# Performance work log

Measured on AMD Instinct MI355X. Metric: run time of the kernel, lower is better.

The kernel has to match this reference:

```python
import jax, jax.numpy as jnp
import numpy as np

ALPHA = 0.2  # LeakyReLU negative slope for GAT attention
NEG_INF = -1e9


def setup_inputs() -> dict:
    key = jax.random.key(0)
    ks = jax.random.split(key, 10)
    B, N = 8, 1024
    D_vis, D_lab = 512, 256
    H, F = 8, 64            # n_heads, out_per_head -> gat output dim 512
    D_in = D_vis + D_lab    # 768
    D_gat = H * F           # 512
    D_emb = 512

    visual_features = jax.random.normal(ks[0], (B, D_vis), dtype=jnp.float32)
    labels_features = jax.random.normal(ks[1], (N, D_lab), dtype=jnp.float32)
    adj = (jax.random.uniform(ks[2], (N, N)) < 0.1).astype(jnp.float32)
    label_adj_matrix = jnp.maximum(adj, jnp.eye(N, dtype=jnp.float32))

    s = 1.0 / np.sqrt(D_in)
    W = jax.random.uniform(ks[3], (D_in, H, F), minval=-s, maxval=s, dtype=jnp.float32)
    sa = 1.0 / np.sqrt(F)
    a_src = jax.random.uniform(ks[4], (H, F), minval=-sa, maxval=sa, dtype=jnp.float32)
    a_dst = jax.random.uniform(ks[5], (H, F), minval=-sa, maxval=sa, dtype=jnp.float32)
    sq = 1.0 / np.sqrt(D_gat)
    pool_q = jax.random.uniform(ks[6], (D_gat,), minval=-sq, maxval=sq, dtype=jnp.float32)
    fc_W = jax.random.uniform(ks[7], (D_gat, D_emb), minval=-sq, maxval=sq, dtype=jnp.float32)
    fc_b = jax.random.uniform(ks[8], (D_emb,), minval=-sq, maxval=sq, dtype=jnp.float32)

    return {
        "visual_features": visual_features,
        "labels_features": labels_features,
        "label_adj_matrix": label_adj_matrix,
        "W": W, "a_src": a_src, "a_dst": a_dst,
        "pool_q": pool_q, "fc_W": fc_W, "fc_b": fc_b,
    }


def gat_layer(x, adj, W, a_src, a_dst):
    """Multi-head GAT (concat heads). x: (B,N,Din), adj: (N,N)."""
    B, N, _ = x.shape
    H, F = a_src.shape
    Wh = jnp.einsum('bni,ihf->bnhf', x, W)              # (B,N,H,F)
    e_src = jnp.einsum('bnhf,hf->bnh', Wh, a_src)       # (B,N,H)
    e_dst = jnp.einsum('bnhf,hf->bnh', Wh, a_dst)       # (B,N,H)
    e = e_src[:, :, None, :] + e_dst[:, None, :, :]     # (B,N,N,H)
    e = jnp.where(e > 0, e, ALPHA * e)                  # LeakyReLU
    mask = (adj > 0)[None, :, :, None]                  # (1,N,N,1)
    e = jnp.where(mask, e, NEG_INF)
    att = jax.nn.softmax(e, axis=2)                     # over neighbors j
    out = jnp.einsum('bnjh,bjhf->bnhf', att, Wh)        # aggregate
    out = out.reshape(B, N, H * F)
    return jax.nn.elu(out)                              # concat_heads=True -> elu


def reference(visual_features, labels_features, label_adj_matrix,
              W, a_src, a_dst, pool_q, fc_W, fc_b):
    B = visual_features.shape[0]
    N = labels_features.shape[0]
    # per-batch node features: [label_feat || global visual feat]
    lab = jnp.broadcast_to(labels_features[None], (B, N, labels_features.shape[1]))
    vis = jnp.broadcast_to(visual_features[:, None, :], (B, N, visual_features.shape[1]))
    x = jnp.concatenate([lab, vis], axis=-1)            # (B,N,D_in)

    x = gat_layer(x, label_adj_matrix, W, a_src, a_dst) # (B,N,H*F)

    # attention pooling over nodes
    scores = jnp.einsum('bnd,d->bn', x, pool_q)         # (B,N)
    w = jax.nn.softmax(scores, axis=1)
    pooled = jnp.einsum('bn,bnd->bd', w, x)             # (B,D_gat)

    return pooled @ fc_W + fc_b                         # (B,final_embedding_dim)
```

## Files before the change

### kernel.cpp

```cpp
#include <hip/hip_runtime.h>
#include <hip/hip_bf16.h>

#define NN 1024
#define BB 8
#define HH 8
#define FF 64
#define HF 512
#define KT 128

typedef unsigned short ushortT;

__device__ __forceinline__ ushortT f2bf(float f) {
    __hip_bfloat16 h = __float2bfloat16(f);
    return *(ushortT*)&h;
}
__device__ __forceinline__ float bf2f_u(ushortT u) {
    return __uint_as_float((unsigned)u << 16);
}

__global__ void __launch_bounds__(256) k_prep(
    const float* __restrict__ lab, const float* __restrict__ vis,
    const float* __restrict__ adj, const float* __restrict__ Wm,
    const float* __restrict__ a_src, const float* __restrict__ a_dst,
    ushortT* __restrict__ whb, float* __restrict__ whv2, float* __restrict__ bvp,
    float* __restrict__ es, float* __restrict__ ed, float* __restrict__ edT,
    int* __restrict__ list, int* __restrict__ cnt, float* __restrict__ outp)
{
    int bx = blockIdx.x, t = threadIdx.x;
    __shared__ float sh[1024];
    __shared__ float whs[1024];
    if (bx < 512) {
        int np = bx >> 1, ch = bx & 1, n0 = np * 4;
        #pragma unroll
        for (int nd = 0; nd < 4; ++nd)
            sh[nd * 256 + t] = lab[(n0 + nd) * 256 + t];
        __syncthreads();
        float a0 = 0.f, a1 = 0.f, a2 = 0.f, a3 = 0.f;
        const float* wp = Wm + ch * 256 + t;
        #pragma unroll 8
        for (int i = 0; i < 256; ++i) {
            float w = wp[(size_t)i * HF];
            a0 += sh[i] * w;
            a1 += sh[256 + i] * w;
            a2 += sh[512 + i] * w;
            a3 += sh[768 + i] * w;
        }
        int cb = ch * 256 + t;
        whb[(size_t)(n0 + 0) * HF + cb] = f2bf(a0);
        whb[(size_t)(n0 + 1) * HF + cb] = f2bf(a1);
        whb[(size_t)(n0 + 2) * HF + cb] = f2bf(a2);
        whb[(size_t)(n0 + 3) * HF + cb] = f2bf(a3);
        whs[t] = a0; whs[256 + t] = a1; whs[512 + t] = a2; whs[768 + t] = a3;
        __syncthreads();
        if (t < 32) {
            int nd = t >> 3, rest = t & 7, hl = rest >> 1, sd = rest & 1;
            int h = ch * 4 + hl;
            const float* av = (sd ? a_dst : a_src) + h * FF;
            const float* wr = whs + nd * 256 + hl * FF;
            float s = 0.f;
            #pragma unroll
            for (int f = 0; f < FF; ++f) s += wr[f] * av[f];
            int n = n0 + nd;
            if (sd) { ed[n * HH + h] = s; edT[h * NN + n] = s; }
            else es[n * HH + h] = s;
        }
    } else if (bx < 528) {
        int id = bx - 512, b = id >> 1, kh = id & 1;
        if (t < 256) sh[t] = vis[b * 512 + kh * 256 + t];
        __syncthreads();
        float a0 = 0.f, a1 = 0.f;
        const float* wp = Wm + (size_t)(256 + kh * 256) * HF;
        #pragma unroll 4
        for (int i = 0; i < 256; ++i) {
            float xv = sh[i];
            a0 += xv * wp[(size_t)i * HF + t];
            a1 += xv * wp[(size_t)i * HF + t + 256];
        }
        float* dst = whv2 + (size_t)(kh * BB + b) * HF;
        dst[t] = a0; dst[t + 256] = a1;
        whs[t] = a0; whs[256 + t] = a1;
        __syncthreads();
        if (t < 8) {
            const float* as = a_src + t * FF;
            const float* ad = a_dst + t * FF;
            const float* wr = whs + t * FF;
            float s = 0.f;
            #pragma unroll 8
            for (int f = 0; f < FF; ++f) s += wr[f] * (as[f] + ad[f]);
            bvp[kh * 64 + b * 8 + t] = s;
        }
    } else if (bx < 784) {
        int id = bx - 528;
        int i = id * 4 + (t >> 6), lane = t & 63;
        int base = 0;
        for (int c = 0; c < 16; ++c) {
            int j = c * 64 + lane;
            bool pres = adj[(size_t)i * NN + j] > 0.f;
            unsigned long long m = __ballot(pres);
            int pos = __popcll(m & ((1ull << lane) - 1ull));
            if (pres) list[i * NN + base + pos] = j;
            base += __popcll(m);
        }
        if (lane == 0) cnt[i] = base;
    } else {
        float4 z; z.x = 0.f; z.y = 0.f; z.z = 0.f; z.w = 0.f;
        float4* oo = (float4*)outp;
        #pragma unroll
        for (int q = 0; q < 4; ++q) oo[q * 256 + t] = z;
    }
}

__global__ void __launch_bounds__(256) k_attn(
    const ushortT* __restrict__ whb, const float* __restrict__ whv2,
    const float* __restrict__ es, const float* __restrict__ ed,
    const float* __restrict__ edT, const float* __restrict__ bvp,
    const int* __restrict__ list, const int* __restrict__ cnt,
    const float* __restrict__ pool_q,
    ushortT* __restrict__ xoutb, float* __restrict__ sch)
{
    int i = blockIdx.x, z = blockIdx.y, t = threadIdx.x;
    int nn = cnt[i];

    __shared__ float att[KT * 32];
    __shared__ int jl[KT];
    __shared__ float base_s[32], M_s[32], inv_s[32];
    __shared__ float red[8][32];
    __shared__ float edmax_z[4];

    {
        int hl = t >> 6, h = z * 4 + hl;
        const float* col = edT + h * NN;
        float m = -1e30f;
        #pragma unroll
        for (int g = 0; g < 16; ++g) m = fmaxf(m, col[(t & 63) + g * 64]);
        #pragma unroll
        for (int off = 32; off > 0; off >>= 1) m = fmaxf(m, __shfl_down(m, off));
        if ((t & 63) == 0) edmax_z[hl] = m;
    }
    __syncthreads();
    if (t < 32) {
        int hl = t >> 3, b = t & 7, h = z * 4 + hl;
        float base = es[i * HH + h] + bvp[b * 8 + h] + bvp[64 + b * 8 + h];
        base_s[t] = base;
        float mv = base + edmax_z[hl];
        M_s[t] = mv > 0.f ? mv : 0.2f * mv;
    }
    __syncthreads();

    int p = t & 31;
    int hp = z * 4 + (p >> 3);
    float basev = base_s[p], Mv = M_s[p];
    float ssum = 0.f;

    int wid = t >> 6, tf = t & 63;
    int f0 = z * 256 + 4 * tf;
    int hl8 = (tf >> 4) * 8;
    float ac[32];
    #pragma unroll
    for (int q = 0; q < 32; ++q) ac[q] = 0.f;

    for (int c0 = 0; c0 < nn; c0 += KT) {
        int kc = min(KT, nn - c0);
        __syncthreads();
        if (t < kc) jl[t] = list[(size_t)i * NN + c0 + t];
        __syncthreads();
        for (int k = t >> 5; k < kc; k += 8) {
            int j = jl[k];
            float e = basev + ed[j * HH + hp];
            e = e > 0.f ? e : 0.2f * e;
            float pe = __expf(e - Mv);
            ssum += pe;
            att[k * 32 + p] = pe;
        }
        __syncthreads();
        {
            ushort4 u0; u0.x = 0; u0.y = 0; u0.z = 0; u0.w = 0;
            ushort4 u1 = u0;
            if (wid < kc)     u0 = *(const ushort4*)&whb[(size_t)jl[wid] * HF + f0];
            if (wid + 4 < kc) u1 = *(const ushort4*)&whb[(size_t)jl[wid + 4] * HF + f0];
            for (int k = wid; k < kc; k += 4) {
                ushort4 u2 = u1;
                if (k + 8 < kc) u2 = *(const ushort4*)&whb[(size_t)jl[k + 8] * HF + f0];
                float r0 = bf2f_u(u0.x), r1 = bf2f_u(u0.y);
                float r2 = bf2f_u(u0.z), r3 = bf2f_u(u0.w);
                const float4 aA = *(const float4*)&att[k * 32 + hl8];
                const float4 aB = *(const float4*)&att[k * 32 + hl8 + 4];
                ac[0]  += aA.x * r0; ac[8]  += aA.x * r1; ac[16] += aA.x * r2; ac[24] += aA.x * r3;
                ac[1]  += aA.y * r0; ac[9]  += aA.y * r1; ac[17] += aA.y * r2; ac[25] += aA.y * r3;
                ac[2]  += aA.z * r0; ac[10] += aA.z * r1; ac[18] += aA.z * r2; ac[26] += aA.z * r3;
                ac[3]  += aA.w * r0; ac[11] += aA.w * r1; ac[19] += aA.w * r2; ac[27] += aA.w * r3;
                ac[4]  += aB.x * r0; ac[12] += aB.x * r1; ac[20] += aB.x * r2; ac[28] += aB.x * r3;
                ac[5]  += aB.y * r0; ac[13] += aB.y * r1; ac[21] += aB.y * r2; ac[29] += aB.y * r3;
                ac[6]  += aB.z * r0; ac[14] += aB.z * r1; ac[22] += aB.z * r2; ac[30] += aB.z * r3;
                ac[7]  += aB.w * r0; ac[15] += aB.w * r1; ac[23] += aB.w * r2; ac[31] += aB.w * r3;
                u0 = u1; u1 = u2;
            }
        }
    }

    __syncthreads();
    red[t >> 5][p] = ssum;
    float* mrg = att;
    if (wid == 3) {
        #pragma unroll
        for (int q = 0; q < 32; ++q) mrg[q * 64 + tf] = ac[q];
    }
    __syncthreads();
    if (t < 32) {
        float s = 0.f;
        #pragma unroll
        for (int g = 0; g < 8; ++g) s += red[g][t];
        inv_s[t] = 1.0f / s;
    }
    if (wid == 2) {
        #pragma unroll
        for (int q = 0; q < 32; ++q) mrg[q * 64 + tf] += ac[q];
    }
    __syncthreads();
    if (wid == 1) {
        #pragma unroll
        for (int q = 0; q < 32; ++q) mrg[q * 64 + tf] += ac[q];
    }
    __syncthreads();

    if (wid == 0) {
        #pragma unroll
        for (int q = 0; q < 32; ++q) ac[q] += mrg[q * 64 + tf];
        int hl = tf >> 4;
        const float4 pq4 = *(const float4*)&pool_q[f0];
        #pragma unroll
        for (int b = 0; b < BB; ++b) {
            float iv = inv_s[hl * 8 + b];
            const float4 wva = *(const float4*)&whv2[(size_t)b * HF + f0];
            const float4 wvb = *(const float4*)&whv2[(size_t)(BB + b) * HF + f0];
            float o0 = ac[b]      * iv + wva.x + wvb.x;
            float o1 = ac[8 + b]  * iv + wva.y + wvb.y;
            float o2 = ac[16 + b] * iv + wva.z + wvb.z;
            float o3 = ac[24 + b] * iv + wva.w + wvb.w;
            o0 = o0 > 0.f ? o0 : (__expf(o0) - 1.f);
            o1 = o1 > 0.f ? o1 : (__expf(o1) - 1.f);
            o2 = o2 > 0.f ? o2 : (__expf(o2) - 1.f);
            o3 = o3 > 0.f ? o3 : (__expf(o3) - 1.f);
            ushort4 ov;
            ov.x = f2bf(o0); ov.y = f2bf(o1); ov.z = f2bf(o2); ov.w = f2bf(o3);
            *(ushort4*)&xoutb[((size_t)b * NN + i) * HF + f0] = ov;
            float sp = o0 * pq4.x + o1 * pq4.y + o2 * pq4.z + o3 * pq4.w;
            #pragma unroll
            for (int off = 32; off > 0; off >>= 1) sp += __shfl_down(sp, off);
            if (t == 0) sch[(z * BB + b) * NN + i] = sp;
        }
    }
}

__global__ void __launch_bounds__(256) k_tail(const float* __restrict__ sch,
    const ushortT* __restrict__ xoutb, const float* __restrict__ fcW,
    const float* __restrict__ fcb, float* __restrict__ out)
{
    int q = blockIdx.x, b = blockIdx.y, t = threadIdx.x;
    int lane = t & 63, wid = t >> 6;
    __shared__ float red[4];
    __shared__ float sM, sI;
    __shared__ float wl[NN];
    __shared__ float part[16][16];
    __shared__ float pl[16];

    float v[4], e[4];
    float mx = -1e30f;
    #pragma unroll
    for (int qq = 0; qq < 4; ++qq) {
        int n = qq * 256 + t;
        v[qq] = sch[b * NN + n] + sch[(BB + b) * NN + n];
        mx = fmaxf(mx, v[qq]);
    }
    #pragma unroll
    for (int off = 32; off > 0; off >>= 1) mx = fmaxf(mx, __shfl_down(mx, off));
    if (lane == 0) red[wid] = mx;
    __syncthreads();
    if (t == 0) sM = fmaxf(fmaxf(red[0], red[1]), fmaxf(red[2], red[3]));
    __syncthreads();
    float sMv = sM;
    float sm = 0.f;
    #pragma unroll
    for (int qq = 0; qq < 4; ++qq) { e[qq] = __expf(v[qq] - sMv); sm += e[qq]; }
    #pragma unroll
    for (int off = 32; off > 0; off >>= 1) sm += __shfl_down(sm, off);
    __syncthreads();
    if (lane == 0) red[wid] = sm;
    __syncthreads();
    if (t == 0) sI = 1.0f / (red[0] + red[1] + red[2] + red[3]);
    __syncthreads();
    float sIv = sI;
    #pragma unroll
    for (int qq = 0; qq < 4; ++qq) wl[qq * 256 + t] = e[qq] * sIv;
    __syncthreads();

    int fl = t & 15, ng = t >> 4;
    const ushortT* xb = xoutb + (size_t)b * NN * HF + q * 16 + fl;
    float acc0 = 0.f, acc1 = 0.f;
    #pragma unroll 8
    for (int n0 = 0; n0 < NN; n0 += 32) {
        int na = n0 + ng, nb2 = n0 + 16 + ng;
        acc0 += wl[na]  * bf2f_u(xb[(size_t)na  * HF]);
        acc1 += wl[nb2] * bf2f_u(xb[(size_t)nb2 * HF]);
    }
    part[ng][fl] = acc0 + acc1;
    __syncthreads();
    if (t < 16) {
        float s = 0.f;
        #pragma unroll
        for (int g = 0; g < 16; ++g) s += part[g][t];
        pl[t] = s;
    }
    __syncthreads();

    int f0 = 2 * t;
    float ax = 0.f, ay = 0.f;
    if (q == 0) { ax = fcb[f0]; ay = fcb[f0 + 1]; }
    #pragma unroll
    for (int kk = 0; kk < 16; ++kk) {
        float pv = pl[kk];
        const float2 w2 = *(const float2*)&fcW[(size_t)(q * 16 + kk) * HF + f0];
        ax += pv * w2.x; ay += pv * w2.y;
    }
    atomicAdd(&out[b * HF + f0], ax);
    atomicAdd(&out[b * HF + f0 + 1], ay);
}

extern "C" void kernel_launch(void* const* d_in, const int* in_sizes, int n_in,
                              void* d_out, int out_size, void* d_ws, size_t ws_size,
                              hipStream_t stream) {
    const float* vis   = (const float*)d_in[0];
    const float* lab   = (const float*)d_in[1];
    const float* adj   = (const float*)d_in[2];
    const float* Wm    = (const float*)d_in[3];
    const float* a_src = (const float*)d_in[4];
    const float* a_dst = (const float*)d_in[5];
    const float* pq    = (const float*)d_in[6];
    const float* fcW   = (const float*)d_in[7];
    const float* fcb   = (const float*)d_in[8];
    float* out = (float*)d_out;

    char* w = (char*)d_ws;
    ushortT* whb  = (ushortT*)w; w += (size_t)NN * HF * 2;
    float* whv2   = (float*)w;   w += (size_t)2 * BB * HF * 4;
    float* bvp    = (float*)w;   w += 2 * 64 * 4;
    float* es     = (float*)w;   w += (size_t)NN * HH * 4;
    float* ed     = (float*)w;   w += (size_t)NN * HH * 4;
    float* edT    = (float*)w;   w += (size_t)HH * NN * 4;
    int*   nlist  = (int*)w;     w += (size_t)NN * NN * 4;
    int*   ncnt   = (int*)w;     w += (size_t)NN * 4;
    ushortT* xoutb = (ushortT*)w; w += (size_t)BB * NN * HF * 2;
    float* sch    = (float*)w;   w += (size_t)2 * BB * NN * 4;

    k_prep<<<785, 256, 0, stream>>>(lab, vis, adj, Wm, a_src, a_dst,
                                    whb, whv2, bvp, es, ed, edT, nlist, ncnt, out);
    k_attn<<<dim3(NN, 2), 256, 0, stream>>>(whb, whv2, es, ed, edT, bvp,
                                            nlist, ncnt, pq, xoutb, sch);
    k_tail<<<dim3(32, BB), 256, 0, stream>>>(sch, xoutb, fcW, fcb, out);
}
```

Baseline: 75.40 us.

## Stage neighbor Wh rows and ed values in shared memory for aggregation

Gathered bf16 Wh rows for each 32-neighbor sub-batch are now loaded cooperatively by all threads into a shared-memory tile. The aggregation loop then reads from that tile instead of issuing per-thread global gathers with a manual software prefetch. The per-neighbor ed values are also gathered once per chunk as float4 into shared memory, which removes redundant global reads in the exp loop. In exchange the kernel takes extra barriers per sub-batch and uses more shared memory, which may lower occupancy.

After: 79.17 us. 5.0% more time.

```diff
diff --git a/kernel.cpp b/kernel.cpp
--- a/kernel.cpp
+++ b/kernel.cpp
@@ -122,6 +122,8 @@
     int nn = cnt[i];
 
     __shared__ float att[KT * 32];
+    __shared__ ushortT whs[32 * 256];
+    __shared__ float edl[KT * 4];
     __shared__ int jl[KT];
     __shared__ float base_s[32], M_s[32], inv_s[32];
     __shared__ float red[8][32];
@@ -148,7 +150,6 @@
     __syncthreads();
 
     int p = t & 31;
-    int hp = z * 4 + (p >> 3);
     float basev = base_s[p], Mv = M_s[p];
     float ssum = 0.f;
 
@@ -162,29 +163,39 @@
     for (int c0 = 0; c0 < nn; c0 += KT) {
         int kc = min(KT, nn - c0);
         __syncthreads();
-        if (t < kc) jl[t] = list[(size_t)i * NN + c0 + t];
+        if (t < kc) {
+            int jv = list[(size_t)i * NN + c0 + t];
+            jl[t] = jv;
+            float4 v = *(const float4*)&ed[(size_t)jv * HH + z * 4];
+            *(float4*)&edl[t * 4] = v;
+        }
         __syncthreads();
         for (int k = t >> 5; k < kc; k += 8) {
-            int j = jl[k];
-            float e = basev + ed[j * HH + hp];
+            float e = basev + edl[(k << 2) + (p >> 3)];
             e = e > 0.f ? e : 0.2f * e;
             float pe = __expf(e - Mv);
             ssum += pe;
             att[k * 32 + p] = pe;
         }
-        __syncthreads();
-        {
-            ushort4 u0; u0.x = 0; u0.y = 0; u0.z = 0; u0.w = 0;
-            ushort4 u1 = u0;
-            if (wid < kc)     u0 = *(const ushort4*)&whb[(size_t)jl[wid] * HF + f0];
-            if (wid + 4 < kc) u1 = *(const ushort4*)&whb[(size_t)jl[wid + 4] * HF + f0];
-            for (int k = wid; k < kc; k += 4) {
-                ushort4 u2 = u1;
-                if (k + 8 < kc) u2 = *(const ushort4*)&whb[(size_t)jl[k + 8] * HF + f0];
-                float r0 = bf2f_u(u0.x), r1 = bf2f_u(u0.y);
-                float r2 = bf2f_u(u0.z), r3 = bf2f_u(u0.w);
-                const float4 aA = *(const float4*)&att[k * 32 + hl8];
-                const float4 aB = *(const float4*)&att[k * 32 + hl8 + 4];
+        for (int b0 = 0; b0 < kc; b0 += 32) {
+            int bcnt = min(32, kc - b0);
+            __syncthreads();
+            #pragma unroll
+            for (int r = 0; r < 8; ++r) {
+                int idx = r * 256 + t;
+                int row = idx >> 6, c4 = idx & 63;
+                if (row < bcnt) {
+                    ushort4 u = *(const ushort4*)&whb[(size_t)jl[b0 + row] * HF + z * 256 + c4 * 4];
+                    *(ushort4*)&whs[row * 256 + c4 * 4] = u;
+                }
+            }
+            __syncthreads();
+            for (int k = wid; k < bcnt; k += 4) {
+                const ushort4 u = *(const ushort4*)&whs[k * 256 + 4 * tf];
+                float r0 = bf2f_u(u.x), r1 = bf2f_u(u.y);
+                float r2 = bf2f_u(u.z), r3 = bf2f_u(u.w);
+                const float4 aA = *(const float4*)&att[(b0 + k) * 32 + hl8];
+                const float4 aB = *(const float4*)&att[(b0 + k) * 32 + hl8 + 4];
                 ac[0]  += aA.x * r0; ac[8]  += aA.x * r1; ac[16] += aA.x * r2; ac[24] += aA.x * r3;
                 ac[1]  += aA.y * r0; ac[9]  += aA.y * r1; ac[17] += aA.y * r2; ac[25] += aA.y * r3;
                 ac[2]  += aA.z * r0; ac[10] += aA.z * r1; ac[18] += aA.z * r2; ac[26] += aA.z * r3;
@@ -193,7 +204,6 @@
                 ac[5]  += aB.y * r0; ac[13] += aB.y * r1; ac[21] += aB.y * r2; ac[29] += aB.y * r3;
                 ac[6]  += aB.z * r0; ac[14] += aB.z * r1; ac[22] += aB.z * r2; ac[30] += aB.z * r3;
                 ac[7]  += aB.w * r0; ac[15] += aB.w * r1; ac[23] += aB.w * r2; ac[31] += aB.w * r3;
-                u0 = u1; u1 = u2;
             }
         }
     }
```
